# Kernel tuning notes

Measured on AMD Instinct MI355X. Metric: run time of the kernel, lower is better.

Reference implementation:

```python
import jax, jax.numpy as jnp
import numpy as np

B, L, D, H = 2, 128, 256, 256
BASE_LR = 0.01
LR_SHIFT = float(np.log(np.expm1(BASE_LR)))  # log(expm1(base_lr))


def silu_backward(x):
    s = jax.nn.silu(x)
    return s + jax.nn.sigmoid(x) * (1.0 - s)


def decay_matrix(log_g):
    # log_g: [B,L] -> M[b,l,m] = exp(sum_{i=m+1..l} log_g[b,i]) for m<=l, else 0
    n = log_g.shape[1]
    strict = jnp.tril(jnp.ones((n, n), log_g.dtype), -1)
    cum = jnp.cumsum(log_g[:, :, None] * strict, axis=1)
    return jnp.exp(cum) * jnp.tril(jnp.ones((n, n), log_g.dtype))


def setup_inputs():
    key = jax.random.key(0)
    ks = jax.random.split(key, 22)
    p = lambda k, shape: jax.random.normal(k, shape, jnp.float32) * 0.02
    inp = {
        'x': jax.random.normal(ks[0], (B, L, D), jnp.float32),
        'Wq': p(ks[1], (D, D)), 'bq': p(ks[2], (D,)),
        'Wk': p(ks[3], (D, D)), 'bk': p(ks[4], (D,)),
        'Wv': p(ks[5], (D, D)), 'bv': p(ks[6], (D,)),
        'Wlr': p(ks[7], (D, 1)), 'blr': p(ks[8], (1,)),
        'Wm': p(ks[9], (D, 1)), 'bm': p(ks[10], (1,)),
        'Wd': p(ks[11], (D, 1)), 'bd': p(ks[12], (1,)),
        'W1': p(ks[13], (B, H, D)), 'b1': p(ks[14], (B, H)),
        'W2': p(ks[15], (B, D, H)), 'b2': p(ks[16], (B, D)),
        'mW1': p(ks[17], (B, H, D)), 'mb1': p(ks[18], (B, H)),
        'mW2': p(ks[19], (B, D, H)), 'mb2': p(ks[20], (B, D)),
    }
    return inp


def reference(x, Wq, bq, Wk, bk, Wv, bv, Wlr, blr, Wm, bm, Wd, bd,
              W1, b1, W2, b2, mW1, mb1, mW2, mb2):
    query = x @ Wq + bq
    key_ = x @ Wk + bk
    value = x @ Wv + bv

    # forward through fast-weight MLP at current (chunk-start) weights
    Z1 = jnp.einsum('bhd,bld->blh', W1, key_) + b1[:, None, :]
    X2 = jax.nn.silu(Z1)
    Z2 = jnp.einsum('bdh,blh->bld', W2, X2) + b2[:, None, :]

    # per-token gradients of 0.5*||Z2 - value||^2
    grad_Z2 = Z2 - value
    grad_b2 = grad_Z2
    grad_W2 = jnp.einsum('bld,blh->bldh', grad_Z2, X2)
    grad_X2 = jnp.einsum('bld,bdh->blh', grad_Z2, W2)
    grad_Z1 = grad_X2 * silu_backward(Z1)
    grad_b1 = grad_Z1
    grad_W1 = jnp.einsum('blh,bld->blhd', grad_Z1, key_)

    lr = jax.nn.softplus((x @ Wlr).squeeze(-1) + blr + LR_SHIFT)  # [B,L]
    gW1 = grad_W1 * lr[:, :, None, None]
    gb1 = grad_b1 * lr[:, :, None]
    gW2 = grad_W2 * lr[:, :, None, None]
    gb2 = grad_b2 * lr[:, :, None]

    # momentum recurrence (decay-gated linear scan, materialized as LxL matrix)
    fc_mom = (x @ Wm).squeeze(-1) + bm  # [B,L]
    log_mom = -jax.nn.softplus(-fc_mom)
    M = decay_matrix(log_mom)  # [B,L,L]
    mom_cum = jnp.exp(jnp.cumsum(log_mom, axis=1))  # [B,L]

    mgW1 = jnp.einsum('blm,bmhd->blhd', M, gW1) - jnp.einsum('bl,bhd->blhd', mom_cum, mW1)
    mgb1 = jnp.einsum('blm,bmh->blh', M, gb1) - jnp.einsum('bl,bh->blh', mom_cum, mb1)
    mgW2 = jnp.einsum('blm,bmdh->bldh', M, gW2) - jnp.einsum('bl,bdh->bldh', mom_cum, mW2)
    mgb2 = jnp.einsum('blm,bmd->bld', M, gb2) - jnp.einsum('bl,bd->bld', mom_cum, mb2)

    # weight-decay recurrence
    log_wd = -jax.nn.softplus((x @ Wd).squeeze(-1) + bd)  # [B,L]
    Dm = decay_matrix(log_wd)
    wd_cum = jnp.exp(jnp.cumsum(log_wd, axis=1))

    W1p = jnp.einsum('blm,bmhd->blhd', Dm, mgW1) + jnp.einsum('bl,bhd->blhd', wd_cum, W1)
    b1p = jnp.einsum('blm,bmh->blh', Dm, mgb1) + jnp.einsum('bl,bh->blh', wd_cum, b1)
    W2p = jnp.einsum('blm,bmdh->bldh', Dm, mgW2) + jnp.einsum('bl,bdh->bldh', wd_cum, W2)
    b2p = jnp.einsum('blm,bmd->bld', Dm, mgb2) + jnp.einsum('bl,bd->bld', wd_cum, b2)

    # query pass through per-token updated weights
    Zq1 = jnp.einsum('blhd,bld->blh', W1p, query) + b1p
    Zq2 = jnp.einsum('bldh,blh->bld', W2p, jax.nn.silu(Zq1)) + b2p

    return (Zq2,
            W1p[:, -1], b1p[:, -1], W2p[:, -1], b2p[:, -1],
            mgW1[:, -1], mgb1[:, -1], mgW2[:, -1], mgb2[:, -1])
```

## Files before the change

kernel.cpp:

```cpp
#include <hip/hip_runtime.h>
#include <math.h>

constexpr int Bn = 2, Ln = 128, Dn = 256, Hn = 256;

#define LR_SHIFT (-4.6001660040607144f)

constexpr int OFF_Q      = 0;
constexpr int OFF_K      = 65536;
constexpr int OFF_V      = 131072;
constexpr int OFF_X2     = 196608;
constexpr int OFF_GZ1    = 262144;
constexpr int OFF_GZ2    = 327680;
constexpr int OFF_XQ     = 393216;
constexpr int OFF_KT     = 458752;
constexpr int OFF_A      = 524288;
constexpr int OFF_W1T    = 557056;
constexpr int OFF_W2T    = 688128;
constexpr int OFF_MW1T   = 819200;
constexpr int OFF_MW2T   = 950272;
constexpr int OFF_LR     = 1081344;
constexpr int OFF_PM     = 1081600;
constexpr int OFF_PD     = 1081856;
constexpr int OFF_MOMCUM = 1082112;
constexpr int OFF_WDCUM  = 1082368;
constexpr int OFF_C      = 1082624;
constexpr int OFF_LOGM   = 1082880;
constexpr int OFF_LOGWD  = 1083136;
constexpr int OFF_X2T    = 1083392;
constexpr int OFF_U1     = 1148928;
constexpr int OFF_V1     = 1214464;
constexpr int OFF_U2     = 1280000;
constexpr int OFF_V2     = 1345536;
constexpr int OFF_P2     = OFF_V;

constexpr int OUT_ZQ2  = 0;
constexpr int OUT_W1P  = 65536;
constexpr int OUT_B1P  = 196608;
constexpr int OUT_W2P  = 197120;
constexpr int OUT_B2P  = 328192;
constexpr int OUT_MGW1 = 328704;
constexpr int OUT_MGB1 = 459776;
constexpr int OUT_MGW2 = 460288;
constexpr int OUT_MGB2 = 591360;

__device__ __forceinline__ float softplus_f(float z) {
    return fmaxf(z, 0.0f) + log1pf(expf(-fabsf(z)));
}

__device__ __forceinline__ float4 fma4(float s, const float4 w, float4 a) {
    a.x += s * w.x; a.y += s * w.y; a.z += s * w.z; a.w += s * w.w; return a;
}

__device__ __forceinline__ float silu_f(float z) {
    return z / (1.0f + expf(-z));
}

__device__ __forceinline__ float dsilu_mul(float a, float z) {
    float sg = 1.0f / (1.0f + expf(-z));
    return a * (sg * (1.0f + z * (1.0f - sg)));
}

__device__ __forceinline__ void gemm_tile_16x128(
    const float* __restrict__ srcrow,
    const float* __restrict__ W,
    const float* __restrict__ bias,
    float* __restrict__ dst,
    int c0, int t, float* smem) {
    float (*xs)[260] = (float (*)[260])smem;
    for (int i = t; i < 1024; i += 256) {
        int tok = i >> 6, kq = i & 63;
        *(float4*)&xs[tok][kq * 4] = *(const float4*)(srcrow + tok * 256 + kq * 4);
    }
    __syncthreads();
    int tg = t >> 5, q = t & 31;
    int tok0 = 2 * tg, tok1 = tok0 + 1;
    int c = c0 + 4 * q;
    const float* Wp = W + c;
    float4 a0 = {0, 0, 0, 0}, a1 = {0, 0, 0, 0};
    for (int k0 = 0; k0 < 256; k0 += 16) {
        float4 wb[16];
#pragma unroll
        for (int kk = 0; kk < 16; ++kk)
            wb[kk] = *(const float4*)(Wp + (k0 + kk) * 256);
#pragma unroll
        for (int kk = 0; kk < 16; ++kk) {
            a0 = fma4(xs[tok0][k0 + kk], wb[kk], a0);
            a1 = fma4(xs[tok1][k0 + kk], wb[kk], a1);
        }
    }
    if (bias) {
        float4 bb = *(const float4*)(bias + c);
        a0.x += bb.x; a0.y += bb.y; a0.z += bb.z; a0.w += bb.w;
        a1.x += bb.x; a1.y += bb.y; a1.z += bb.z; a1.w += bb.w;
    }
    *(float4*)(dst + tok0 * 256 + c) = a0;
    *(float4*)(dst + tok1 * 256 + c) = a1;
}

__global__ __launch_bounds__(256) void prep_kernel(
    const float* __restrict__ x,
    const float* __restrict__ Wq, const float* __restrict__ bq,
    const float* __restrict__ Wk, const float* __restrict__ bk,
    const float* __restrict__ Wv, const float* __restrict__ bv,
    const float* __restrict__ Wlr, const float* __restrict__ blr,
    const float* __restrict__ Wm, const float* __restrict__ bm,
    const float* __restrict__ Wd, const float* __restrict__ bd,
    const float* __restrict__ W1, const float* __restrict__ W2,
    const float* __restrict__ mW1, const float* __restrict__ mW2,
    float* __restrict__ ws) {
    __shared__ float smem[4160];
    int id = blockIdx.x, t = threadIdx.x;
    if (id < 512) {
        int z = id >> 6; int mat = z >> 1; int b = z & 1;
        const float* src; float* dst;
        if (mat == 0)      { src = W1  + b * 65536; dst = ws + OFF_W1T  + b * 65536; }
        else if (mat == 1) { src = W2  + b * 65536; dst = ws + OFF_W2T  + b * 65536; }
        else if (mat == 2) { src = mW1 + b * 65536; dst = ws + OFF_MW1T + b * 65536; }
        else               { src = mW2 + b * 65536; dst = ws + OFF_MW2T + b * 65536; }
        float (*tile)[33] = (float (*)[33])smem;
        int tx = t & 31, ty = t >> 5;
        int tid = id & 63;
        int r0 = (tid >> 3) * 32, c0 = (tid & 7) * 32;
        for (int i = 0; i < 32; i += 8)
            tile[ty + i][tx] = src[(r0 + ty + i) * 256 + (c0 + tx)];
        __syncthreads();
        for (int i = 0; i < 32; i += 8)
            dst[(c0 + ty + i) * 256 + (r0 + tx)] = tile[tx][ty + i];
    } else if (id < 608) {
        int u = id - 512; int mat = u >> 5; int rem = u & 31;
        int c0 = (rem >> 4) * 128; int bl0 = (rem & 15) * 16;
        const float* W    = (mat == 0) ? Wq : (mat == 1) ? Wk : Wv;
        const float* bias = (mat == 0) ? bq : (mat == 1) ? bk : bv;
        int outoff = (mat == 0) ? OFF_Q : (mat == 1) ? OFF_K : OFF_V;
        gemm_tile_16x128(x + bl0 * 256, W, bias, ws + outoff + bl0 * 256, c0, t, smem);
    } else {
        int blk = id - 608;
        int ln = t & 63, wv = t >> 6;
        int bl = blk * 4 + wv;
        float4 xv = *(const float4*)(x + bl * 256 + ln * 4);
        float4 wl = *(const float4*)(Wlr + ln * 4);
        float4 wm = *(const float4*)(Wm + ln * 4);
        float4 wd = *(const float4*)(Wd + ln * 4);
        float s1 = xv.x * wl.x + xv.y * wl.y + xv.z * wl.z + xv.w * wl.w;
        float s2 = xv.x * wm.x + xv.y * wm.y + xv.z * wm.z + xv.w * wm.w;
        float s3 = xv.x * wd.x + xv.y * wd.y + xv.z * wd.z + xv.w * wd.w;
#pragma unroll
        for (int off = 32; off > 0; off >>= 1) {
            s1 += __shfl_xor(s1, off);
            s2 += __shfl_xor(s2, off);
            s3 += __shfl_xor(s3, off);
        }
        if (ln == 0) {
            ws[OFF_LR + bl]    = softplus_f(s1 + blr[0] + LR_SHIFT);
            ws[OFF_LOGM + bl]  = -softplus_f(-(s2 + bm[0]));
            ws[OFF_LOGWD + bl] = -softplus_f(s3 + bd[0]);
        }
    }
}

__global__ __launch_bounds__(256) void mid_kernel(
    const float* __restrict__ W2nat, const float* __restrict__ b1,
    const float* __restrict__ b2, const float* __restrict__ mb1,
    float* __restrict__ ws) {
    __shared__ float smem[8320];
    int id = blockIdx.x, t = threadIdx.x;
    if (id < 32) {
        int bl0 = id * 8;
        int b = bl0 >> 7;
        float (*ks)[260] = (float (*)[260])smem;
        float (*zs)[260] = (float (*)[260])(smem + 2080);
        float (*as)[260] = (float (*)[260])(smem + 4160);
        float (*gs)[260] = (float (*)[260])(smem + 6240);
        for (int i = t; i < 512; i += 256) {
            int tok = i >> 6, kq = i & 63;
            *(float4*)&ks[tok][kq * 4] =
                *(const float4*)(ws + OFF_K + (bl0 + tok) * 256 + kq * 4);
        }
        __syncthreads();
        int tok = t >> 5, q = t & 31;
        int c = 4 * q, c2 = c + 128;
        {
            const float* W1t = ws + OFF_W1T + b * 65536;
            float4 a0 = {0, 0, 0, 0}, a1 = {0, 0, 0, 0};
            for (int k0 = 0; k0 < 256; k0 += 8) {
                float4 w0[8], w1[8];
#pragma unroll
                for (int kk = 0; kk < 8; ++kk) {
                    w0[kk] = *(const float4*)(W1t + (k0 + kk) * 256 + c);
                    w1[kk] = *(const float4*)(W1t + (k0 + kk) * 256 + c2);
                }
#pragma unroll
                for (int kk = 0; kk < 8; ++kk) {
                    float kv = ks[tok][k0 + kk];
                    a0 = fma4(kv, w0[kk], a0);
                    a1 = fma4(kv, w1[kk], a1);
                }
            }
            float4 bb0 = *(const float4*)(b1 + b * 256 + c);
            float4 bb1 = *(const float4*)(b1 + b * 256 + c2);
            float4 z0 = {a0.x + bb0.x, a0.y + bb0.y, a0.z + bb0.z, a0.w + bb0.w};
            float4 z1 = {a1.x + bb1.x, a1.y + bb1.y, a1.z + bb1.z, a1.w + bb1.w};
            *(float4*)&zs[tok][c]  = z0;
            *(float4*)&zs[tok][c2] = z1;
            float4 s0 = {silu_f(z0.x), silu_f(z0.y), silu_f(z0.z), silu_f(z0.w)};
            float4 s1 = {silu_f(z1.x), silu_f(z1.y), silu_f(z1.z), silu_f(z1.w)};
            *(float4*)&as[tok][c]  = s0;
            *(float4*)&as[tok][c2] = s1;
            *(float4*)(ws + OFF_X2 + (bl0 + tok) * 256 + c)  = s0;
            *(float4*)(ws + OFF_X2 + (bl0 + tok) * 256 + c2) = s1;
        }
        __syncthreads();
        {
            int l0b = bl0 & 127;
            float v0[8], v1[8];
#pragma unroll
            for (int j = 0; j < 8; ++j) { v0[j] = ks[j][t]; v1[j] = as[j][t]; }
            float* KTp  = ws + OFF_KT  + b * 32768 + t * 128 + l0b;
            float* X2Tp = ws + OFF_X2T + b * 32768 + t * 128 + l0b;
            float4 p0 = {v0[0], v0[1], v0[2], v0[3]};
            float4 p1 = {v0[4], v0[5], v0[6], v0[7]};
            *(float4*)KTp = p0; *(float4*)(KTp + 4) = p1;
            float4 r0 = {v1[0], v1[1], v1[2], v1[3]};
            float4 r1 = {v1[4], v1[5], v1[6], v1[7]};
            *(float4*)X2Tp = r0; *(float4*)(X2Tp + 4) = r1;
        }
        {
            const float* W2t = ws + OFF_W2T + b * 65536;
            float4 a0 = {0, 0, 0, 0}, a1 = {0, 0, 0, 0};
            for (int k0 = 0; k0 < 256; k0 += 8) {
                float4 w0[8], w1[8];
#pragma unroll
                for (int kk = 0; kk < 8; ++kk) {
                    w0[kk] = *(const float4*)(W2t + (k0 + kk) * 256 + c);
                    w1[kk] = *(const float4*)(W2t + (k0 + kk) * 256 + c2);
                }
#pragma unroll
                for (int kk = 0; kk < 8; ++kk) {
                    float xv = as[tok][k0 + kk];
                    a0 = fma4(xv, w0[kk], a0);
                    a1 = fma4(xv, w1[kk], a1);
                }
            }
            float4 bb0 = *(const float4*)(b2 + b * 256 + c);
            float4 bb1 = *(const float4*)(b2 + b * 256 + c2);
            float4 v0 = *(const float4*)(ws + OFF_V + (bl0 + tok) * 256 + c);
            float4 v1 = *(const float4*)(ws + OFF_V + (bl0 + tok) * 256 + c2);
            float4 g0 = {a0.x + bb0.x - v0.x, a0.y + bb0.y - v0.y,
                         a0.z + bb0.z - v0.z, a0.w + bb0.w - v0.w};
            float4 g1 = {a1.x + bb1.x - v1.x, a1.y + bb1.y - v1.y,
                         a1.z + bb1.z - v1.z, a1.w + bb1.w - v1.w};
            *(float4*)&gs[tok][c]  = g0;
            *(float4*)&gs[tok][c2] = g1;
            *(float4*)(ws + OFF_GZ2 + (bl0 + tok) * 256 + c)  = g0;
            *(float4*)(ws + OFF_GZ2 + (bl0 + tok) * 256 + c2) = g1;
        }
        __syncthreads();
        {
            const float* W2n = W2nat + b * 65536;
            float4 a0 = {0, 0, 0, 0}, a1 = {0, 0, 0, 0};
            for (int k0 = 0; k0 < 256; k0 += 8) {
                float4 w0[8], w1[8];
#pragma unroll
                for (int kk = 0; kk < 8; ++kk) {
                    w0[kk] = *(const float4*)(W2n + (k0 + kk) * 256 + c);
                    w1[kk] = *(const float4*)(W2n + (k0 + kk) * 256 + c2);
                }
#pragma unroll
                for (int kk = 0; kk < 8; ++kk) {
                    float gv = gs[tok][k0 + kk];
                    a0 = fma4(gv, w0[kk], a0);
                    a1 = fma4(gv, w1[kk], a1);
                }
            }
            float4 z0 = *(float4*)&zs[tok][c];
            float4 z1 = *(float4*)&zs[tok][c2];
            float4 g0 = {dsilu_mul(a0.x, z0.x), dsilu_mul(a0.y, z0.y),
                         dsilu_mul(a0.z, z0.z), dsilu_mul(a0.w, z0.w)};
            float4 g1 = {dsilu_mul(a1.x, z1.x), dsilu_mul(a1.y, z1.y),
                         dsilu_mul(a1.z, z1.z), dsilu_mul(a1.w, z1.w)};
            *(float4*)(ws + OFF_GZ1 + (bl0 + tok) * 256 + c)  = g0;
            *(float4*)(ws + OFF_GZ1 + (bl0 + tok) * 256 + c2) = g1;
        }
    } else if (id < 288) {
        int u = id - 32; int b = u >> 7; int l = u & 127;
        float* sm = smem;
        float* sd = smem + 128;
        float* se = smem + 256;
        if (t < 128) {
            sm[t] = ws[OFF_LOGM + b * Ln + t];
            sd[t] = ws[OFF_LOGWD + b * Ln + t];
        }
        __syncthreads();
        for (int off = 1; off < 128; off <<= 1) {
            float am = 0.0f, ad = 0.0f;
            if (t < 128 && t >= off) { am = sm[t - off]; ad = sd[t - off]; }
            __syncthreads();
            if (t < 128) { sm[t] += am; sd[t] += ad; }
            __syncthreads();
        }
        if (l == 0) {
            if (t < 128) {
                float pm = sm[t], pd = sd[t];
                ws[OFF_PM + b * Ln + t] = pm;
                ws[OFF_PD + b * Ln + t] = pd;
                ws[OFF_MOMCUM + b * Ln + t] = expf(pm);
                ws[OFF_WDCUM + b * Ln + t]  = expf(pd);
                se[t] = expf(pm - pd);
            }
            __syncthreads();
            for (int off = 1; off < 128; off <<= 1) {
                float a = 0.0f;
                if (t < 128 && t >= off) a = se[t - off];
                __syncthreads();
                if (t < 128) se[t] += a;
                __syncthreads();
            }
            if (t < 128) ws[OFF_C + b * Ln + t] = expf(sd[t]) * se[t];
        }
        if (t < 128) {
            int m1 = t;
            float a = 0.0f;
            if (m1 <= l) {
                float pdl = sd[l], pmm1 = sm[m1];
                float s = 0.0f;
                for (int m = m1; m <= l; ++m)
                    s += expf((pdl - sd[m]) + (sm[m] - pmm1));
                a = s;
            }
            ws[OFF_A + (b * Ln + l) * Ln + m1] = a;
        }
    } else {
        int u = id - 288; int mat = u >> 5; int rem = u & 31;
        int c0 = (rem >> 4) * 128; int bl0 = (rem & 15) * 16;
        int b = bl0 >> 7;
        const float* W    = ws + (mat == 0 ? OFF_W1T : OFF_MW1T) + b * 65536;
        const float* bias = (mat == 0 ? b1 : mb1) + b * 256;
        float* dst = ws + (mat == 0 ? OFF_U1 : OFF_V1) + bl0 * 256;
        gemm_tile_16x128(ws + OFF_Q + bl0 * 256, W, bias, dst, c0, t, smem);
    }
}

__global__ __launch_bounds__(256) void fin1_kernel(
    const float* __restrict__ W1, const float* __restrict__ mW1,
    const float* __restrict__ W2nat, const float* __restrict__ mW2,
    const float* __restrict__ b1, const float* __restrict__ mb1,
    const float* __restrict__ b2, const float* __restrict__ mb2,
    float* __restrict__ out, float* __restrict__ ws) {
    __shared__ float smem[6400];
    int id = blockIdx.x, t = threadIdx.x;
    if (id < 64) {
        int b = id >> 5; int rem = id & 31;
        int l0 = (rem >> 1) * 8; int ct = rem & 1;
        int bl0 = b * 128 + l0; int c0 = ct * 128;
        float (*qs)[260] = (float (*)[260])smem;
        float (*ps)[132] = (float (*)[132])(smem + 2080);
        for (int i = t; i < 512; i += 256) {
            int tok = i >> 6, kq = i & 63;
            *(float4*)&qs[tok][kq * 4] =
                *(const float4*)(ws + OFF_Q + (bl0 + tok) * 256 + kq * 4);
        }
        __syncthreads();
        int tok = t >> 5;
        int l = l0 + tok;
        {
            int mq = t & 31, m0 = 4 * mq;
            const float* KT = ws + OFF_KT + b * 32768 + m0;
            float4 s = {0, 0, 0, 0};
            for (int d0 = 0; d0 < 256; d0 += 16) {
                float4 kb[16];
#pragma unroll
                for (int kk = 0; kk < 16; ++kk)
                    kb[kk] = *(const float4*)(KT + (d0 + kk) * 128);
#pragma unroll
                for (int kk = 0; kk < 16; ++kk)
                    s = fma4(qs[tok][d0 + kk], kb[kk], s);
            }
            float4 A4 = *(const float4*)(ws + OFF_A + (b * 128 + l) * 128 + m0);
            float4 L4 = *(const float4*)(ws + OFF_LR + b * 128 + m0);
            float4 pv;
            pv.x = (m0 + 0 <= l) ? A4.x * L4.x * (1.0f + s.x) : 0.0f;
            pv.y = (m0 + 1 <= l) ? A4.y * L4.y * (1.0f + s.y) : 0.0f;
            pv.z = (m0 + 2 <= l) ? A4.z * L4.z * (1.0f + s.z) : 0.0f;
            pv.w = (m0 + 3 <= l) ? A4.w * L4.w * (1.0f + s.w) : 0.0f;
            *(float4*)&ps[tok][m0] = pv;
        }
        __syncthreads();
        {
            int q = t & 31;
            int c = c0 + 4 * q;
            float cl  = ws[OFF_C + b * 128 + l];
            float wdc = ws[OFF_WDCUM + b * 128 + l];
            float4 p = {0, 0, 0, 0};
            const float* G = ws + OFF_GZ1 + b * 32768 + c;
            int mmax = l0 + 8;
            for (int m0 = 0; m0 < mmax; m0 += 8) {
                float4 gb[8];
#pragma unroll
                for (int kk = 0; kk < 8; ++kk)
                    gb[kk] = *(const float4*)(G + (m0 + kk) * 256);
#pragma unroll
                for (int kk = 0; kk < 8; ++kk)
                    p = fma4(ps[tok][m0 + kk], gb[kk], p);
            }
            float4 u4 = *(const float4*)(ws + OFF_U1 + (bl0 + tok) * 256 + c);
            float4 v4 = *(const float4*)(ws + OFF_V1 + (bl0 + tok) * 256 + c);
            float4 o;
            o.x = silu_f(p.x - cl * v4.x + wdc * u4.x);
            o.y = silu_f(p.y - cl * v4.y + wdc * u4.y);
            o.z = silu_f(p.z - cl * v4.z + wdc * u4.z);
            o.w = silu_f(p.w - cl * v4.w + wdc * u4.w);
            *(float4*)(ws + OFF_XQ + (bl0 + tok) * 256 + c) = o;
        }
    } else if (id < 1088) {
        int u = id - 64; int z = u >> 8; int rem = u & 255;
        int b = z >> 1; int fam = z & 1;
        int i0 = (rem >> 4) * 16, j0 = (rem & 15) * 16;
        float* wa = smem;
        float* wm = smem + 128;
        float (*LA)[16] = (float (*)[16])(smem + 256);
        float (*LM)[16] = (float (*)[16])(smem + 256 + 2048);
        float (*R)[16]  = (float (*)[16])(smem + 256 + 4096);
        const float* lr = ws + OFF_LR + b * Ln;
        const float* Pm = ws + OFF_PM + b * Ln;
        const float* Arow = ws + OFF_A + (b * Ln + Ln - 1) * Ln;
        if (t < 128) {
            wa[t] = Arow[t] * lr[t];
            wm[t] = expf(Pm[Ln - 1] - Pm[t]) * lr[t];
        }
        const float* left  = ws + (fam == 0 ? OFF_GZ1 : OFF_GZ2) + b * Ln * 256;
        const float* right = ws + (fam == 0 ? OFF_K   : OFF_X2 ) + b * Ln * 256;
        __syncthreads();
        for (int e = t; e < 2048; e += 256) {
            int m = e >> 4, i = e & 15;
            float lv = left[m * 256 + i0 + i];
            LA[m][i] = wa[m] * lv;
            LM[m][i] = wm[m] * lv;
            R[m][i]  = right[m * 256 + j0 + i];
        }
        __syncthreads();
        int tx = t & 15, ty = t >> 4;
        float accA = 0.0f, accM = 0.0f;
#pragma unroll 4
        for (int m = 0; m < 128; ++m) {
            accA += LA[m][ty] * R[m][tx];
            accM += LM[m][ty] * R[m][tx];
        }
        float c_last  = ws[OFF_C + b * Ln + Ln - 1];
        float wd_last = ws[OFF_WDCUM + b * Ln + Ln - 1];
        float mc_last = ws[OFF_MOMCUM + b * Ln + Ln - 1];
        int i = i0 + ty, j = j0 + tx;
        const float* base1 = (fam == 0 ? W1 : W2nat) + b * 65536;
        const float* basem = (fam == 0 ? mW1 : mW2) + b * 65536;
        float b1v = base1[i * 256 + j], bmv = basem[i * 256 + j];
        int op = (fam == 0 ? OUT_W1P : OUT_W2P) + (b * 256 + i) * 256 + j;
        int om = (fam == 0 ? OUT_MGW1 : OUT_MGW2) + (b * 256 + i) * 256 + j;
        out[op] = accA - c_last * bmv + wd_last * b1v;
        out[om] = accM - mc_last * bmv;
    } else {
        int b = id - 1088;
        float* wa = smem;
        float* wm = smem + 128;
        if (t < 128) {
            wa[t] = ws[OFF_A + (b * Ln + Ln - 1) * Ln + t] * ws[OFF_LR + b * Ln + t];
            wm[t] = expf(ws[OFF_PM + b * Ln + Ln - 1] - ws[OFF_PM + b * Ln + t]) *
                    ws[OFF_LR + b * Ln + t];
        }
        __syncthreads();
        const float* gz1 = ws + OFF_GZ1 + b * Ln * 256;
        const float* gz2 = ws + OFF_GZ2 + b * Ln * 256;
        float sA1 = 0, sM1 = 0, sA2 = 0, sM2 = 0;
#pragma unroll 4
        for (int m = 0; m < 128; ++m) {
            float g1 = gz1[m * 256 + t], g2 = gz2[m * 256 + t];
            sA1 += wa[m] * g1; sM1 += wm[m] * g1;
            sA2 += wa[m] * g2; sM2 += wm[m] * g2;
        }
        float c_last  = ws[OFF_C + b * Ln + Ln - 1];
        float wd_last = ws[OFF_WDCUM + b * Ln + Ln - 1];
        float mc_last = ws[OFF_MOMCUM + b * Ln + Ln - 1];
        out[OUT_B1P + b * 256 + t]  = sA1 - c_last * mb1[b * 256 + t] + wd_last * b1[b * 256 + t];
        out[OUT_MGB1 + b * 256 + t] = sM1 - mc_last * mb1[b * 256 + t];
        out[OUT_B2P + b * 256 + t]  = sA2 - c_last * mb2[b * 256 + t] + wd_last * b2[b * 256 + t];
        out[OUT_MGB2 + b * 256 + t] = sM2 - mc_last * mb2[b * 256 + t];
    }
}

__global__ __launch_bounds__(256) void fin2_kernel(
    const float* __restrict__ b2, const float* __restrict__ mb2,
    float* __restrict__ ws) {
    __shared__ float smem[4160];
    int id = blockIdx.x, t = threadIdx.x;
    if (id < 32) {
        int b = id >> 4; int l0 = (id & 15) * 8; int bl0 = b * 128 + l0;
        float (*qs)[260] = (float (*)[260])smem;
        for (int i = t; i < 512; i += 256) {
            int tok = i >> 6, kq = i & 63;
            *(float4*)&qs[tok][kq * 4] =
                *(const float4*)(ws + OFF_XQ + (bl0 + tok) * 256 + kq * 4);
        }
        __syncthreads();
        int tok = t >> 5, mq = t & 31, m0 = 4 * mq;
        int l = l0 + tok;
        const float* X2T = ws + OFF_X2T + b * 32768 + m0;
        float4 s = {0, 0, 0, 0};
        for (int d0 = 0; d0 < 256; d0 += 16) {
            float4 kb[16];
#pragma unroll
            for (int kk = 0; kk < 16; ++kk)
                kb[kk] = *(const float4*)(X2T + (d0 + kk) * 128);
#pragma unroll
            for (int kk = 0; kk < 16; ++kk)
                s = fma4(qs[tok][d0 + kk], kb[kk], s);
        }
        float4 A4 = *(const float4*)(ws + OFF_A + (b * 128 + l) * 128 + m0);
        float4 L4 = *(const float4*)(ws + OFF_LR + b * 128 + m0);
        float4 pv;
        pv.x = (m0 + 0 <= l) ? A4.x * L4.x * (1.0f + s.x) : 0.0f;
        pv.y = (m0 + 1 <= l) ? A4.y * L4.y * (1.0f + s.y) : 0.0f;
        pv.z = (m0 + 2 <= l) ? A4.z * L4.z * (1.0f + s.z) : 0.0f;
        pv.w = (m0 + 3 <= l) ? A4.w * L4.w * (1.0f + s.w) : 0.0f;
        *(float4*)(ws + OFF_P2 + (b * 128 + l) * 128 + m0) = pv;
    } else {
        int u = id - 32; int mat = u >> 5; int rem = u & 31;
        int c0 = (rem >> 4) * 128; int bl0 = (rem & 15) * 16;
        int b = bl0 >> 7;
        const float* W    = ws + (mat == 0 ? OFF_W2T : OFF_MW2T) + b * 65536;
        const float* bias = (mat == 0 ? b2 : mb2) + b * 256;
        float* dst = ws + (mat == 0 ? OFF_U2 : OFF_V2) + bl0 * 256;
        gemm_tile_16x128(ws + OFF_XQ + bl0 * 256, W, bias, dst, c0, t, smem);
    }
}

__global__ __launch_bounds__(256) void fin3_kernel(
    float* __restrict__ out, float* __restrict__ ws) {
    __shared__ float smem[1056];
    int id = blockIdx.x, t = threadIdx.x;
    int b = id >> 5; int rem = id & 31;
    int l0 = (rem >> 1) * 8; int ct = rem & 1;
    int bl0 = b * 128 + l0; int c0 = ct * 128;
    float (*ps)[132] = (float (*)[132])smem;
    {
        int tok = t >> 5, mq = t & 31;
        *(float4*)&ps[tok][mq * 4] =
            *(const float4*)(ws + OFF_P2 + (b * 128 + l0 + tok) * 128 + mq * 4);
    }
    __syncthreads();
    int tok = t >> 5, q = t & 31;
    int l = l0 + tok;
    int c = c0 + 4 * q;
    float cl  = ws[OFF_C + b * 128 + l];
    float wdc = ws[OFF_WDCUM + b * 128 + l];
    float4 p = {0, 0, 0, 0};
    const float* G = ws + OFF_GZ2 + b * 32768 + c;
    int mmax = l0 + 8;
    for (int m0 = 0; m0 < mmax; m0 += 8) {
        float4 gb[8];
#pragma unroll
        for (int kk = 0; kk < 8; ++kk)
            gb[kk] = *(const float4*)(G + (m0 + kk) * 256);
#pragma unroll
        for (int kk = 0; kk < 8; ++kk)
            p = fma4(ps[tok][m0 + kk], gb[kk], p);
    }
    float4 u4 = *(const float4*)(ws + OFF_U2 + (bl0 + tok) * 256 + c);
    float4 v4 = *(const float4*)(ws + OFF_V2 + (bl0 + tok) * 256 + c);
    float4 o;
    o.x = p.x - cl * v4.x + wdc * u4.x;
    o.y = p.y - cl * v4.y + wdc * u4.y;
    o.z = p.z - cl * v4.z + wdc * u4.z;
    o.w = p.w - cl * v4.w + wdc * u4.w;
    *(float4*)(out + OUT_ZQ2 + (bl0 + tok) * 256 + c) = o;
}

extern "C" void kernel_launch(void* const* d_in, const int* in_sizes, int n_in,
                              void* d_out, int out_size, void* d_ws, size_t ws_size,
                              hipStream_t stream) {
    const float* x   = (const float*)d_in[0];
    const float* Wq  = (const float*)d_in[1];
    const float* bq  = (const float*)d_in[2];
    const float* Wk  = (const float*)d_in[3];
    const float* bk  = (const float*)d_in[4];
    const float* Wv  = (const float*)d_in[5];
    const float* bv  = (const float*)d_in[6];
    const float* Wlr = (const float*)d_in[7];
    const float* blr = (const float*)d_in[8];
    const float* Wm  = (const float*)d_in[9];
    const float* bm  = (const float*)d_in[10];
    const float* Wd  = (const float*)d_in[11];
    const float* bd  = (const float*)d_in[12];
    const float* W1  = (const float*)d_in[13];
    const float* b1  = (const float*)d_in[14];
    const float* W2  = (const float*)d_in[15];
    const float* b2  = (const float*)d_in[16];
    const float* mW1 = (const float*)d_in[17];
    const float* mb1 = (const float*)d_in[18];
    const float* mW2 = (const float*)d_in[19];
    const float* mb2 = (const float*)d_in[20];
    float* ws  = (float*)d_ws;
    float* out = (float*)d_out;

    prep_kernel<<<672, 256, 0, stream>>>(x, Wq, bq, Wk, bk, Wv, bv,
                                         Wlr, blr, Wm, bm, Wd, bd,
                                         W1, W2, mW1, mW2, ws);
    mid_kernel<<<352, 256, 0, stream>>>(W2, b1, b2, mb1, ws);
    fin1_kernel<<<1090, 256, 0, stream>>>(W1, mW1, W2, mW2,
                                          b1, mb1, b2, mb2, out, ws);
    fin2_kernel<<<96, 256, 0, stream>>>(b2, mb2, ws);
    fin3_kernel<<<64, 256, 0, stream>>>(out, ws);
}
```

Before: 216.4 us.

## Replace five-kernel pipeline with cooperative persistent megakernel using grid syncs

Merges the separate prep/mid/fin kernels into a single persistent cooperative kernel that walks seven phases, with grid-wide synchronisation between them. Work is redistributed into per-phase units (score, combine, last-weight, bias reductions) over a grid capped by occupancy. The goal is to remove launch overhead and tail idle time between the five launches. The cost is grid-sync latency, lower parallelism per phase, and a fallback that launches the kernel once per phase when cooperative launch is unavailable.

```diff
diff --git a/kernel.cpp b/kernel.cpp
--- a/kernel.cpp
+++ b/kernel.cpp
@@ -1,5 +1,8 @@
 #include <hip/hip_runtime.h>
+#include <hip/hip_cooperative_groups.h>
 #include <math.h>
+
+namespace cg = cooperative_groups;
 
 constexpr int Bn = 2, Ln = 128, Dn = 256, Hn = 256;
 
@@ -31,6 +34,7 @@
 constexpr int OFF_V1     = 1214464;
 constexpr int OFF_U2     = 1280000;
 constexpr int OFF_V2     = 1345536;
+constexpr int OFF_P1     = 1411072;
 constexpr int OFF_P2     = OFF_V;
 
 constexpr int OUT_ZQ2  = 0;
@@ -43,506 +47,129 @@
 constexpr int OUT_MGW2 = 460288;
 constexpr int OUT_MGB2 = 591360;
 
+struct KParams {
+    const float *x;
+    const float *Wq, *bq, *Wk, *bk, *Wv, *bv;
+    const float *Wlr, *blr, *Wm, *bm, *Wd, *bd;
+    const float *W1, *b1, *W2, *b2, *mW1, *mb1, *mW2, *mb2;
+    float *out, *ws;
+};
+
 __device__ __forceinline__ float softplus_f(float z) {
     return fmaxf(z, 0.0f) + log1pf(expf(-fabsf(z)));
 }
-
 __device__ __forceinline__ float4 fma4(float s, const float4 w, float4 a) {
     a.x += s * w.x; a.y += s * w.y; a.z += s * w.z; a.w += s * w.w; return a;
 }
-
 __device__ __forceinline__ float silu_f(float z) {
     return z / (1.0f + expf(-z));
 }
-
 __device__ __forceinline__ float dsilu_mul(float a, float z) {
     float sg = 1.0f / (1.0f + expf(-z));
     return a * (sg * (1.0f + z * (1.0f - sg)));
 }
 
-__device__ __forceinline__ void gemm_tile_16x128(
-    const float* __restrict__ srcrow,
-    const float* __restrict__ W,
-    const float* __restrict__ bias,
-    float* __restrict__ dst,
-    int c0, int t, float* smem) {
-    float (*xs)[260] = (float (*)[260])smem;
-    for (int i = t; i < 1024; i += 256) {
-        int tok = i >> 6, kq = i & 63;
-        *(float4*)&xs[tok][kq * 4] = *(const float4*)(srcrow + tok * 256 + kq * 4);
-    }
-    __syncthreads();
-    int tg = t >> 5, q = t & 31;
-    int tok0 = 2 * tg, tok1 = tok0 + 1;
-    int c = c0 + 4 * q;
-    const float* Wp = W + c;
-    float4 a0 = {0, 0, 0, 0}, a1 = {0, 0, 0, 0};
+__device__ __forceinline__ void stage8(const float* __restrict__ src,
+                                       float (*xs)[260], int t) {
+#pragma unroll
+    for (int i = 0; i < 2; ++i) {
+        int e = t + i * 256; int tok = e >> 6, kq = e & 63;
+        *(float4*)&xs[tok][kq * 4] = *(const float4*)(src + tok * 256 + kq * 4);
+    }
+}
+
+__device__ __forceinline__ float4 dot256(const float (*xs)[260], int tok,
+                                         const float* __restrict__ Wc, int ldw) {
+    float4 a = {0, 0, 0, 0};
     for (int k0 = 0; k0 < 256; k0 += 16) {
         float4 wb[16];
 #pragma unroll
         for (int kk = 0; kk < 16; ++kk)
-            wb[kk] = *(const float4*)(Wp + (k0 + kk) * 256);
+            wb[kk] = *(const float4*)(Wc + (k0 + kk) * ldw);
 #pragma unroll
-        for (int kk = 0; kk < 16; ++kk) {
-            a0 = fma4(xs[tok0][k0 + kk], wb[kk], a0);
-            a1 = fma4(xs[tok1][k0 + kk], wb[kk], a1);
-        }
-    }
-    if (bias) {
-        float4 bb = *(const float4*)(bias + c);
-        a0.x += bb.x; a0.y += bb.y; a0.z += bb.z; a0.w += bb.w;
-        a1.x += bb.x; a1.y += bb.y; a1.z += bb.z; a1.w += bb.w;
-    }
-    *(float4*)(dst + tok0 * 256 + c) = a0;
-    *(float4*)(dst + tok1 * 256 + c) = a1;
-}
-
-__global__ __launch_bounds__(256) void prep_kernel(
-    const float* __restrict__ x,
-    const float* __restrict__ Wq, const float* __restrict__ bq,
-    const float* __restrict__ Wk, const float* __restrict__ bk,
-    const float* __restrict__ Wv, const float* __restrict__ bv,
-    const float* __restrict__ Wlr, const float* __restrict__ blr,
-    const float* __restrict__ Wm, const float* __restrict__ bm,
-    const float* __restrict__ Wd, const float* __restrict__ bd,
-    const float* __restrict__ W1, const float* __restrict__ W2,
-    const float* __restrict__ mW1, const float* __restrict__ mW2,
-    float* __restrict__ ws) {
-    __shared__ float smem[4160];
-    int id = blockIdx.x, t = threadIdx.x;
-    if (id < 512) {
-        int z = id >> 6; int mat = z >> 1; int b = z & 1;
-        const float* src; float* dst;
-        if (mat == 0)      { src = W1  + b * 65536; dst = ws + OFF_W1T  + b * 65536; }
-        else if (mat == 1) { src = W2  + b * 65536; dst = ws + OFF_W2T  + b * 65536; }
-        else if (mat == 2) { src = mW1 + b * 65536; dst = ws + OFF_MW1T + b * 65536; }
-        else               { src = mW2 + b * 65536; dst = ws + OFF_MW2T + b * 65536; }
-        float (*tile)[33] = (float (*)[33])smem;
-        int tx = t & 31, ty = t >> 5;
-        int tid = id & 63;
-        int r0 = (tid >> 3) * 32, c0 = (tid & 7) * 32;
-        for (int i = 0; i < 32; i += 8)
-            tile[ty + i][tx] = src[(r0 + ty + i) * 256 + (c0 + tx)];
-        __syncthreads();
-        for (int i = 0; i < 32; i += 8)
-            dst[(c0 + ty + i) * 256 + (r0 + tx)] = tile[tx][ty + i];
-    } else if (id < 608) {
-        int u = id - 512; int mat = u >> 5; int rem = u & 31;
-        int c0 = (rem >> 4) * 128; int bl0 = (rem & 15) * 16;
-        const float* W    = (mat == 0) ? Wq : (mat == 1) ? Wk : Wv;
-        const float* bias = (mat == 0) ? bq : (mat == 1) ? bk : bv;
-        int outoff = (mat == 0) ? OFF_Q : (mat == 1) ? OFF_K : OFF_V;
-        gemm_tile_16x128(x + bl0 * 256, W, bias, ws + outoff + bl0 * 256, c0, t, smem);
-    } else {
-        int blk = id - 608;
-        int ln = t & 63, wv = t >> 6;
-        int bl = blk * 4 + wv;
-        float4 xv = *(const float4*)(x + bl * 256 + ln * 4);
-        float4 wl = *(const float4*)(Wlr + ln * 4);
-        float4 wm = *(const float4*)(Wm + ln * 4);
-        float4 wd = *(const float4*)(Wd + ln * 4);
-        float s1 = xv.x * wl.x + xv.y * wl.y + xv.z * wl.z + xv.w * wl.w;
-        float s2 = xv.x * wm.x + xv.y * wm.y + xv.z * wm.z + xv.w * wm.w;
-        float s3 = xv.x * wd.x + xv.y * wd.y + xv.z * wd.z + xv.w * wd.w;
-#pragma unroll
-        for (int off = 32; off > 0; off >>= 1) {
-            s1 += __shfl_xor(s1, off);
-            s2 += __shfl_xor(s2, off);
-            s3 += __shfl_xor(s3, off);
-        }
-        if (ln == 0) {
-            ws[OFF_LR + bl]    = softplus_f(s1 + blr[0] + LR_SHIFT);
-            ws[OFF_LOGM + bl]  = -softplus_f(-(s2 + bm[0]));
-            ws[OFF_LOGWD + bl] = -softplus_f(s3 + bd[0]);
-        }
-    }
-}
-
-__global__ __launch_bounds__(256) void mid_kernel(
-    const float* __restrict__ W2nat, const float* __restrict__ b1,
-    const float* __restrict__ b2, const float* __restrict__ mb1,
-    float* __restrict__ ws) {
-    __shared__ float smem[8320];
-    int id = blockIdx.x, t = threadIdx.x;
-    if (id < 32) {
-        int bl0 = id * 8;
-        int b = bl0 >> 7;
-        float (*ks)[260] = (float (*)[260])smem;
-        float (*zs)[260] = (float (*)[260])(smem + 2080);
-        float (*as)[260] = (float (*)[260])(smem + 4160);
-        float (*gs)[260] = (float (*)[260])(smem + 6240);
-        for (int i = t; i < 512; i += 256) {
-            int tok = i >> 6, kq = i & 63;
-            *(float4*)&ks[tok][kq * 4] =
-                *(const float4*)(ws + OFF_K + (bl0 + tok) * 256 + kq * 4);
-        }
-        __syncthreads();
-        int tok = t >> 5, q = t & 31;
-        int c = 4 * q, c2 = c + 128;
-        {
-            const float* W1t = ws + OFF_W1T + b * 65536;
-            float4 a0 = {0, 0, 0, 0}, a1 = {0, 0, 0, 0};
-            for (int k0 = 0; k0 < 256; k0 += 8) {
-                float4 w0[8], w1[8];
-#pragma unroll
-                for (int kk = 0; kk < 8; ++kk) {
-                    w0[kk] = *(const float4*)(W1t + (k0 + kk) * 256 + c);
-                    w1[kk] = *(const float4*)(W1t + (k0 + kk) * 256 + c2);
-                }
-#pragma unroll
-                for (int kk = 0; kk < 8; ++kk) {
-                    float kv = ks[tok][k0 + kk];
-                    a0 = fma4(kv, w0[kk], a0);
-                    a1 = fma4(kv, w1[kk], a1);
-                }
-            }
-            float4 bb0 = *(const float4*)(b1 + b * 256 + c);
-            float4 bb1 = *(const float4*)(b1 + b * 256 + c2);
-            float4 z0 = {a0.x + bb0.x, a0.y + bb0.y, a0.z + bb0.z, a0.w + bb0.w};
-            float4 z1 = {a1.x + bb1.x, a1.y + bb1.y, a1.z + bb1.z, a1.w + bb1.w};
-            *(float4*)&zs[tok][c]  = z0;
-            *(float4*)&zs[tok][c2] = z1;
-            float4 s0 = {silu_f(z0.x), silu_f(z0.y), silu_f(z0.z), silu_f(z0.w)};
-            float4 s1 = {silu_f(z1.x), silu_f(z1.y), silu_f(z1.z), silu_f(z1.w)};
-            *(float4*)&as[tok][c]  = s0;
-            *(float4*)&as[tok][c2] = s1;
-            *(float4*)(ws + OFF_X2 + (bl0 + tok) * 256 + c)  = s0;
-            *(float4*)(ws + OFF_X2 + (bl0 + tok) * 256 + c2) = s1;
-        }
-        __syncthreads();
-        {
-            int l0b = bl0 & 127;
-            float v0[8], v1[8];
-#pragma unroll
-            for (int j = 0; j < 8; ++j) { v0[j] = ks[j][t]; v1[j] = as[j][t]; }
-            float* KTp  = ws + OFF_KT  + b * 32768 + t * 128 + l0b;
-            float* X2Tp = ws + OFF_X2T + b * 32768 + t * 128 + l0b;
-            float4 p0 = {v0[0], v0[1], v0[2], v0[3]};
-            float4 p1 = {v0[4], v0[5], v0[6], v0[7]};
-            *(float4*)KTp = p0; *(float4*)(KTp + 4) = p1;
-            float4 r0 = {v1[0], v1[1], v1[2], v1[3]};
-            float4 r1 = {v1[4], v1[5], v1[6], v1[7]};
-            *(float4*)X2Tp = r0; *(float4*)(X2Tp + 4) = r1;
-        }
-        {
-            const float* W2t = ws + OFF_W2T + b * 65536;
-            float4 a0 = {0, 0, 0, 0}, a1 = {0, 0, 0, 0};
-            for (int k0 = 0; k0 < 256; k0 += 8) {
-                float4 w0[8], w1[8];
-#pragma unroll
-                for (int kk = 0; kk < 8; ++kk) {
-                    w0[kk] = *(const float4*)(W2t + (k0 + kk) * 256 + c);
-                    w1[kk] = *(const float4*)(W2t + (k0 + kk) * 256 + c2);
-                }
-#pragma unroll
-                for (int kk = 0; kk < 8; ++kk) {
-                    float xv = as[tok][k0 + kk];
-                    a0 = fma4(xv, w0[kk], a0);
-                    a1 = fma4(xv, w1[kk], a1);
-                }
-            }
-            float4 bb0 = *(const float4*)(b2 + b * 256 + c);
-            float4 bb1 = *(const float4*)(b2 + b * 256 + c2);
-            float4 v0 = *(const float4*)(ws + OFF_V + (bl0 + tok) * 256 + c);
-            float4 v1 = *(const float4*)(ws + OFF_V + (bl0 + tok) * 256 + c2);
-            float4 g0 = {a0.x + bb0.x - v0.x, a0.y + bb0.y - v0.y,
-                         a0.z + bb0.z - v0.z, a0.w + bb0.w - v0.w};
-            float4 g1 = {a1.x + bb1.x - v1.x, a1.y + bb1.y - v1.y,
-                         a1.z + bb1.z - v1.z, a1.w + bb1.w - v1.w};
-            *(float4*)&gs[tok][c]  = g0;
-            *(float4*)&gs[tok][c2] = g1;
-            *(float4*)(ws + OFF_GZ2 + (bl0 + tok) * 256 + c)  = g0;
-            *(float4*)(ws + OFF_GZ2 + (bl0 + tok) * 256 + c2) = g1;
-        }
-        __syncthreads();
-        {
-            const float* W2n = W2nat + b * 65536;
-            float4 a0 = {0, 0, 0, 0}, a1 = {0, 0, 0, 0};
-            for (int k0 = 0; k0 < 256; k0 += 8) {
-                float4 w0[8], w1[8];
-#pragma unroll
-                for (int kk = 0; kk < 8; ++kk) {
-                    w0[kk] = *(const float4*)(W2n + (k0 + kk) * 256 + c);
-                    w1[kk] = *(const float4*)(W2n + (k0 + kk) * 256 + c2);
-                }
-#pragma unroll
-                for (int kk = 0; kk < 8; ++kk) {
-                    float gv = gs[tok][k0 + kk];
-                    a0 = fma4(gv, w0[kk], a0);
-                    a1 = fma4(gv, w1[kk], a1);
-                }
-            }
-            float4 z0 = *(float4*)&zs[tok][c];
-            float4 z1 = *(float4*)&zs[tok][c2];
-            float4 g0 = {dsilu_mul(a0.x, z0.x), dsilu_mul(a0.y, z0.y),
-                         dsilu_mul(a0.z, z0.z), dsilu_mul(a0.w, z0.w)};
-            float4 g1 = {dsilu_mul(a1.x, z1.x), dsilu_mul(a1.y, z1.y),
-                         dsilu_mul(a1.z, z1.z), dsilu_mul(a1.w, z1.w)};
-            *(float4*)(ws + OFF_GZ1 + (bl0 + tok) * 256 + c)  = g0;
-            *(float4*)(ws + OFF_GZ1 + (bl0 + tok) * 256 + c2) = g1;
-        }
-    } else if (id < 288) {
-        int u = id - 32; int b = u >> 7; int l = u & 127;
-        float* sm = smem;
-        float* sd = smem + 128;
-        float* se = smem + 256;
-        if (t < 128) {
-            sm[t] = ws[OFF_LOGM + b * Ln + t];
-            sd[t] = ws[OFF_LOGWD + b * Ln + t];
-        }
-        __syncthreads();
-        for (int off = 1; off < 128; off <<= 1) {
-            float am = 0.0f, ad = 0.0f;
-            if (t < 128 && t >= off) { am = sm[t - off]; ad = sd[t - off]; }
-            __syncthreads();
-            if (t < 128) { sm[t] += am; sd[t] += ad; }
-            __syncthreads();
-        }
-        if (l == 0) {
-            if (t < 128) {
-                float pm = sm[t], pd = sd[t];
-                ws[OFF_PM + b * Ln + t] = pm;
-                ws[OFF_PD + b * Ln + t] = pd;
-                ws[OFF_MOMCUM + b * Ln + t] = expf(pm);
-                ws[OFF_WDCUM + b * Ln + t]  = expf(pd);
-                se[t] = expf(pm - pd);
-            }
-            __syncthreads();
-            for (int off = 1; off < 128; off <<= 1) {
-                float a = 0.0f;
-                if (t < 128 && t >= off) a = se[t - off];
-                __syncthreads();
-                if (t < 128) se[t] += a;
-                __syncthreads();
-            }
-            if (t < 128) ws[OFF_C + b * Ln + t] = expf(sd[t]) * se[t];
-        }
-        if (t < 128) {
-            int m1 = t;
-            float a = 0.0f;
-            if (m1 <= l) {
-                float pdl = sd[l], pmm1 = sm[m1];
-                float s = 0.0f;
-                for (int m = m1; m <= l; ++m)
-                    s += expf((pdl - sd[m]) + (sm[m] - pmm1));
-                a = s;
-            }
-            ws[OFF_A + (b * Ln + l) * Ln + m1] = a;
-        }
-    } else {
-        int u = id - 288; int mat = u >> 5; int rem = u & 31;
-        int c0 = (rem >> 4) * 128; int bl0 = (rem & 15) * 16;
-        int b = bl0 >> 7;
-        const float* W    = ws + (mat == 0 ? OFF_W1T : OFF_MW1T) + b * 65536;
-        const float* bias = (mat == 0 ? b1 : mb1) + b * 256;
-        float* dst = ws + (mat == 0 ? OFF_U1 : OFF_V1) + bl0 * 256;
-        gemm_tile_16x128(ws + OFF_Q + bl0 * 256, W, bias, dst, c0, t, smem);
-    }
-}
-
-__global__ __launch_bounds__(256) void fin1_kernel(
-    const float* __restrict__ W1, const float* __restrict__ mW1,
-    const float* __restrict__ W2nat, const float* __restrict__ mW2,
-    const float* __restrict__ b1, const float* __restrict__ mb1,
-    const float* __restrict__ b2, const float* __restrict__ mb2,
-    float* __restrict__ out, float* __restrict__ ws) {
-    __shared__ float smem[6400];
-    int id = blockIdx.x, t = threadIdx.x;
-    if (id < 64) {
-        int b = id >> 5; int rem = id & 31;
-        int l0 = (rem >> 1) * 8; int ct = rem & 1;
-        int bl0 = b * 128 + l0; int c0 = ct * 128;
-        float (*qs)[260] = (float (*)[260])smem;
-        float (*ps)[132] = (float (*)[132])(smem + 2080);
-        for (int i = t; i < 512; i += 256) {
-            int tok = i >> 6, kq = i & 63;
-            *(float4*)&qs[tok][kq * 4] =
-                *(const float4*)(ws + OFF_Q + (bl0 + tok) * 256 + kq * 4);
-        }
-        __syncthreads();
-        int tok = t >> 5;
-        int l = l0 + tok;
-        {
-            int mq = t & 31, m0 = 4 * mq;
-            const float* KT = ws + OFF_KT + b * 32768 + m0;
-            float4 s = {0, 0, 0, 0};
-            for (int d0 = 0; d0 < 256; d0 += 16) {
-                float4 kb[16];
-#pragma unroll
-                for (int kk = 0; kk < 16; ++kk)
-                    kb[kk] = *(const float4*)(KT + (d0 + kk) * 128);
-#pragma unroll
-                for (int kk = 0; kk < 16; ++kk)
-                    s = fma4(qs[tok][d0 + kk], kb[kk], s);
-            }
-            float4 A4 = *(const float4*)(ws + OFF_A + (b * 128 + l) * 128 + m0);
-            float4 L4 = *(const float4*)(ws + OFF_LR + b * 128 + m0);
-            float4 pv;
-            pv.x = (m0 + 0 <= l) ? A4.x * L4.x * (1.0f + s.x) : 0.0f;
-            pv.y = (m0 + 1 <= l) ? A4.y * L4.y * (1.0f + s.y) : 0.0f;
-            pv.z = (m0 + 2 <= l) ? A4.z * L4.z * (1.0f + s.z) : 0.0f;
-            pv.w = (m0 + 3 <= l) ? A4.w * L4.w * (1.0f + s.w) : 0.0f;
-            *(float4*)&ps[tok][m0] = pv;
-        }
-        __syncthreads();
-        {
-            int q = t & 31;
-            int c = c0 + 4 * q;
-            float cl  = ws[OFF_C + b * 128 + l];
-            float wdc = ws[OFF_WDCUM + b * 128 + l];
-            float4 p = {0, 0, 0, 0};
-            const float* G = ws + OFF_GZ1 + b * 32768 + c;
-            int mmax = l0 + 8;
-            for (int m0 = 0; m0 < mmax; m0 += 8) {
-                float4 gb[8];
-#pragma unroll
-                for (int kk = 0; kk < 8; ++kk)
-                    gb[kk] = *(const float4*)(G + (m0 + kk) * 256);
-#pragma unroll
-                for (int kk = 0; kk < 8; ++kk)
-                    p = fma4(ps[tok][m0 + kk], gb[kk], p);
-            }
-            float4 u4 = *(const float4*)(ws + OFF_U1 + (bl0 + tok) * 256 + c);
-            float4 v4 = *(const float4*)(ws + OFF_V1 + (bl0 + tok) * 256 + c);
-            float4 o;
-            o.x = silu_f(p.x - cl * v4.x + wdc * u4.x);
-            o.y = silu_f(p.y - cl * v4.y + wdc * u4.y);
-            o.z = silu_f(p.z - cl * v4.z + wdc * u4.z);
-            o.w = silu_f(p.w - cl * v4.w + wdc * u4.w);
-            *(float4*)(ws + OFF_XQ + (bl0 + tok) * 256 + c) = o;
-        }
-    } else if (id < 1088) {
-        int u = id - 64; int z = u >> 8; int rem = u & 255;
-        int b = z >> 1; int fam = z & 1;
-        int i0 = (rem >> 4) * 16, j0 = (rem & 15) * 16;
-        float* wa = smem;
-        float* wm = smem + 128;
-        float (*LA)[16] = (float (*)[16])(smem + 256);
-        float (*LM)[16] = (float (*)[16])(smem + 256 + 2048);
-        float (*R)[16]  = (float (*)[16])(smem + 256 + 4096);
-        const float* lr = ws + OFF_LR + b * Ln;
-        const float* Pm = ws + OFF_PM + b * Ln;
-        const float* Arow = ws + OFF_A + (b * Ln + Ln - 1) * Ln;
-        if (t < 128) {
-            wa[t] = Arow[t] * lr[t];
-            wm[t] = expf(Pm[Ln - 1] - Pm[t]) * lr[t];
-        }
-        const float* left  = ws + (fam == 0 ? OFF_GZ1 : OFF_GZ2) + b * Ln * 256;
-        const float* right = ws + (fam == 0 ? OFF_K   : OFF_X2 ) + b * Ln * 256;
-        __syncthreads();
-        for (int e = t; e < 2048; e += 256) {
-            int m = e >> 4, i = e & 15;
-            float lv = left[m * 256 + i0 + i];
-            LA[m][i] = wa[m] * lv;
-            LM[m][i] = wm[m] * lv;
-            R[m][i]  = right[m * 256 + j0 + i];
-        }
-        __syncthreads();
-        int tx = t & 15, ty = t >> 4;
-        float accA = 0.0f, accM = 0.0f;
+        for (int kk = 0; kk < 16; ++kk)
+            a = fma4(xs[tok][k0 + kk], wb[kk], a);
+    }
+    return a;
+}
+
+__device__ __forceinline__ void lastw_unit(const KParams& p, float* smem, int t,
+                                           int b, int fam, int i0, int j0) {
+    const float* ws = p.ws;
+    float* wa = smem;
+    float* wm = smem + 128;
+    float (*LA)[16] = (float (*)[16])(smem + 256);
+    float (*LM)[16] = (float (*)[16])(smem + 256 + 2048);
+    float (*R)[16]  = (float (*)[16])(smem + 256 + 4096);
+    const float* lr = ws + OFF_LR + b * Ln;
+    const float* Pm = ws + OFF_PM + b * Ln;
+    const float* Arow = ws + OFF_A + (b * Ln + Ln - 1) * Ln;
+    if (t < 128) {
+        wa[t] = Arow[t] * lr[t];
+        wm[t] = expf(Pm[Ln - 1] - Pm[t]) * lr[t];
+    }
+    const float* left  = ws + (fam == 0 ? OFF_GZ1 : OFF_GZ2) + b * Ln * 256;
+    const float* right = ws + (fam == 0 ? OFF_K   : OFF_X2 ) + b * Ln * 256;
+    __syncthreads();
+    for (int e = t; e < 2048; e += 256) {
+        int m = e >> 4, i = e & 15;
+        float lv = left[m * 256 + i0 + i];
+        LA[m][i] = wa[m] * lv;
+        LM[m][i] = wm[m] * lv;
+        R[m][i]  = right[m * 256 + j0 + i];
+    }
+    __syncthreads();
+    int tx = t & 15, ty = t >> 4;
+    float accA = 0.0f, accM = 0.0f;
 #pragma unroll 4
-        for (int m = 0; m < 128; ++m) {
-            accA += LA[m][ty] * R[m][tx];
-            accM += LM[m][ty] * R[m][tx];
-        }
-        float c_last  = ws[OFF_C + b * Ln + Ln - 1];
-        float wd_last = ws[OFF_WDCUM + b * Ln + Ln - 1];
-        float mc_last = ws[OFF_MOMCUM + b * Ln + Ln - 1];
-        int i = i0 + ty, j = j0 + tx;
-        const float* base1 = (fam == 0 ? W1 : W2nat) + b * 65536;
-        const float* basem = (fam == 0 ? mW1 : mW2) + b * 65536;
-        float b1v = base1[i * 256 + j], bmv = basem[i * 256 + j];
-        int op = (fam == 0 ? OUT_W1P : OUT_W2P) + (b * 256 + i) * 256 + j;
-        int om = (fam == 0 ? OUT_MGW1 : OUT_MGW2) + (b * 256 + i) * 256 + j;
-        out[op] = accA - c_last * bmv + wd_last * b1v;
-        out[om] = accM - mc_last * bmv;
-    } else {
-        int b = id - 1088;
-        float* wa = smem;
-        float* wm = smem + 128;
-        if (t < 128) {
-            wa[t] = ws[OFF_A + (b * Ln + Ln - 1) * Ln + t] * ws[OFF_LR + b * Ln + t];
-            wm[t] = expf(ws[OFF_PM + b * Ln + Ln - 1] - ws[OFF_PM + b * Ln + t]) *
-                    ws[OFF_LR + b * Ln + t];
-        }
-        __syncthreads();
-        const float* gz1 = ws + OFF_GZ1 + b * Ln * 256;
-        const float* gz2 = ws + OFF_GZ2 + b * Ln * 256;
-        float sA1 = 0, sM1 = 0, sA2 = 0, sM2 = 0;
-#pragma unroll 4
-        for (int m = 0; m < 128; ++m) {
-            float g1 = gz1[m * 256 + t], g2 = gz2[m * 256 + t];
-            sA1 += wa[m] * g1; sM1 += wm[m] * g1;
-            sA2 += wa[m] * g2; sM2 += wm[m] * g2;
-        }
-        float c_last  = ws[OFF_C + b * Ln + Ln - 1];
-        float wd_last = ws[OFF_WDCUM + b * Ln + Ln - 1];
-        float mc_last = ws[OFF_MOMCUM + b * Ln + Ln - 1];
-        out[OUT_B1P + b * 256 + t]  = sA1 - c_last * mb1[b * 256 + t] + wd_last * b1[b * 256 + t];
-        out[OUT_MGB1 + b * 256 + t] = sM1 - mc_last * mb1[b * 256 + t];
-        out[OUT_B2P + b * 256 + t]  = sA2 - c_last * mb2[b * 256 + t] + wd_last * b2[b * 256 + t];
-        out[OUT_MGB2 + b * 256 + t] = sM2 - mc_last * mb2[b * 256 + t];
-    }
-}
-
-__global__ __launch_bounds__(256) void fin2_kernel(
-    const float* __restrict__ b2, const float* __restrict__ mb2,
-    float* __restrict__ ws) {
-    __shared__ float smem[4160];
-    int id = blockIdx.x, t = threadIdx.x;
-    if (id < 32) {
-        int b = id >> 4; int l0 = (id & 15) * 8; int bl0 = b * 128 + l0;
-        float (*qs)[260] = (float (*)[260])smem;
-        for (int i = t; i < 512; i += 256) {
-            int tok = i >> 6, kq = i & 63;
-            *(float4*)&qs[tok][kq * 4] =
-                *(const float4*)(ws + OFF_XQ + (bl0 + tok) * 256 + kq * 4);
-        }
-        __syncthreads();
-        int tok = t >> 5, mq = t & 31, m0 = 4 * mq;
-        int l = l0 + tok;
-        const float* X2T = ws + OFF_X2T + b * 32768 + m0;
-        float4 s = {0, 0, 0, 0};
-        for (int d0 = 0; d0 < 256; d0 += 16) {
-            float4 kb[16];
-#pragma unroll
-            for (int kk = 0; kk < 16; ++kk)
-                kb[kk] = *(const float4*)(X2T + (d0 + kk) * 128);
-#pragma unroll
-            for (int kk = 0; kk < 16; ++kk)
-                s = fma4(qs[tok][d0 + kk], kb[kk], s);
-        }
-        float4 A4 = *(const float4*)(ws + OFF_A + (b * 128 + l) * 128 + m0);
-        float4 L4 = *(const float4*)(ws + OFF_LR + b * 128 + m0);
-        float4 pv;
-        pv.x = (m0 + 0 <= l) ? A4.x * L4.x * (1.0f + s.x) : 0.0f;
-        pv.y = (m0 + 1 <= l) ? A4.y * L4.y * (1.0f + s.y) : 0.0f;
-        pv.z = (m0 + 2 <= l) ? A4.z * L4.z * (1.0f + s.z) : 0.0f;
-        pv.w = (m0 + 3 <= l) ? A4.w * L4.w * (1.0f + s.w) : 0.0f;
-        *(float4*)(ws + OFF_P2 + (b * 128 + l) * 128 + m0) = pv;
-    } else {
-        int u = id - 32; int mat = u >> 5; int rem = u & 31;
-        int c0 = (rem >> 4) * 128; int bl0 = (rem & 15) * 16;
-        int b = bl0 >> 7;
-        const float* W    = ws + (mat == 0 ? OFF_W2T : OFF_MW2T) + b * 65536;
-        const float* bias = (mat == 0 ? b2 : mb2) + b * 256;
-        float* dst = ws + (mat == 0 ? OFF_U2 : OFF_V2) + bl0 * 256;
-        gemm_tile_16x128(ws + OFF_XQ + bl0 * 256, W, bias, dst, c0, t, smem);
-    }
-}
-
-__global__ __launch_bounds__(256) void fin3_kernel(
-    float* __restrict__ out, float* __restrict__ ws) {
-    __shared__ float smem[1056];
-    int id = blockIdx.x, t = threadIdx.x;
-    int b = id >> 5; int rem = id & 31;
-    int l0 = (rem >> 1) * 8; int ct = rem & 1;
-    int bl0 = b * 128 + l0; int c0 = ct * 128;
+    for (int m = 0; m < 128; ++m) {
+        accA += LA[m][ty] * R[m][tx];
+        accM += LM[m][ty] * R[m][tx];
+    }
+    float c_last  = ws[OFF_C + b * Ln + Ln - 1];
+    float wd_last = ws[OFF_WDCUM + b * Ln + Ln - 1];
+    float mc_last = ws[OFF_MOMCUM + b * Ln + Ln - 1];
+    int i = i0 + ty, j = j0 + tx;
+    const float* base1 = (fam == 0 ? p.W1 : p.W2) + b * 65536;
+    const float* basem = (fam == 0 ? p.mW1 : p.mW2) + b * 65536;
+    float b1v = base1[i * 256 + j], bmv = basem[i * 256 + j];
+    int op = (fam == 0 ? OUT_W1P : OUT_W2P) + (b * 256 + i) * 256 + j;
+    int om = (fam == 0 ? OUT_MGW1 : OUT_MGW2) + (b * 256 + i) * 256 + j;
+    p.out[op] = accA - c_last * bmv + wd_last * b1v;
+    p.out[om] = accM - mc_last * bmv;
+}
+
+__device__ __forceinline__ void score_unit(const KParams& p, float* smem, int t,
+                                           int b, int l0, int srcoff, int btoff,
+                                           int poff) {
+    const float* ws = p.ws;
+    float (*qs)[260] = (float (*)[260])smem;
+    stage8(ws + srcoff + (b * 128 + l0) * 256, qs, t);
+    __syncthreads();
+    int tok = t >> 5, mq = t & 31, m0 = 4 * mq;
+    int l = l0 + tok;
+    float4 s = dot256(qs, tok, ws + btoff + b * 32768 + m0, 128);
+    float4 A4 = *(const float4*)(ws + OFF_A + (b * 128 + l) * 128 + m0);
+    float4 L4 = *(const float4*)(ws + OFF_LR + b * 128 + m0);
+    float4 pv;
+    pv.x = (m0 + 0 <= l) ? A4.x * L4.x * (1.0f + s.x) : 0.0f;
+    pv.y = (m0 + 1 <= l) ? A4.y * L4.y * (1.0f + s.y) : 0.0f;
+    pv.z = (m0 + 2 <= l) ? A4.z * L4.z * (1.0f + s.z) : 0.0f;
+    pv.w = (m0 + 3 <= l) ? A4.w * L4.w * (1.0f + s.w) : 0.0f;
+    *(float4*)(p.ws + poff + b * 16384 + l * 128 + m0) = pv;
+}
+
+__device__ __forceinline__ void combine_unit(const KParams& p, float* smem, int t,
+                                             int b, int l0, int c0, int poff,
+                                             int goff, int uoff, int voff,
+                                             int dooutsilu, float* dst) {
+    const float* ws = p.ws;
+    int bl0 = b * 128 + l0;
     float (*ps)[132] = (float (*)[132])smem;
     {
         int tok = t >> 5, mq = t & 31;
         *(float4*)&ps[tok][mq * 4] =
-            *(const float4*)(ws + OFF_P2 + (b * 128 + l0 + tok) * 128 + mq * 4);
+            *(const float4*)(ws + poff + b * 16384 + (l0 + tok) * 128 + mq * 4);
     }
     __syncthreads();
     int tok = t >> 5, q = t & 31;
@@ -550,8 +177,8 @@
     int c = c0 + 4 * q;
     float cl  = ws[OFF_C + b * 128 + l];
     float wdc = ws[OFF_WDCUM + b * 128 + l];
-    float4 p = {0, 0, 0, 0};
-    const float* G = ws + OFF_GZ2 + b * 32768 + c;
+    float4 acc = {0, 0, 0, 0};
+    const float* G = ws + goff + b * 32768 + c;
     int mmax = l0 + 8;
     for (int m0 = 0; m0 < mmax; m0 += 8) {
         float4 gb[8];
@@ -560,51 +187,343 @@
             gb[kk] = *(const float4*)(G + (m0 + kk) * 256);
 #pragma unroll
         for (int kk = 0; kk < 8; ++kk)
-            p = fma4(ps[tok][m0 + kk], gb[kk], p);
-    }
-    float4 u4 = *(const float4*)(ws + OFF_U2 + (bl0 + tok) * 256 + c);
-    float4 v4 = *(const float4*)(ws + OFF_V2 + (bl0 + tok) * 256 + c);
+            acc = fma4(ps[tok][m0 + kk], gb[kk], acc);
+    }
+    float4 u4 = *(const float4*)(ws + uoff + (bl0 + tok) * 256 + c);
+    float4 v4 = *(const float4*)(ws + voff + (bl0 + tok) * 256 + c);
     float4 o;
-    o.x = p.x - cl * v4.x + wdc * u4.x;
-    o.y = p.y - cl * v4.y + wdc * u4.y;
-    o.z = p.z - cl * v4.z + wdc * u4.z;
-    o.w = p.w - cl * v4.w + wdc * u4.w;
-    *(float4*)(out + OUT_ZQ2 + (bl0 + tok) * 256 + c) = o;
+    o.x = acc.x - cl * v4.x + wdc * u4.x;
+    o.y = acc.y - cl * v4.y + wdc * u4.y;
+    o.z = acc.z - cl * v4.z + wdc * u4.z;
+    o.w = acc.w - cl * v4.w + wdc * u4.w;
+    if (dooutsilu) {
+        o.x = silu_f(o.x); o.y = silu_f(o.y); o.z = silu_f(o.z); o.w = silu_f(o.w);
+    }
+    *(float4*)(dst + (bl0 + tok) * 256 + c) = o;
+}
+
+__global__ __launch_bounds__(256, 2) void mega_kernel(KParams p, int lo, int hi) {
+    __shared__ float smem[6400];
+    const int t = threadIdx.x;
+    float* ws = p.ws;
+
+    for (int ph = lo; ph <= hi; ++ph) {
+        if (ph > lo) cg::this_grid().sync();
+
+        if (ph == 0) {
+            for (int u = blockIdx.x; u < 768; u += gridDim.x) {
+                if (u < 512) {
+                    int z = u >> 6; int mat = z >> 1; int b = z & 1;
+                    const float* src; float* dst;
+                    if (mat == 0)      { src = p.W1  + b * 65536; dst = ws + OFF_W1T  + b * 65536; }
+                    else if (mat == 1) { src = p.W2  + b * 65536; dst = ws + OFF_W2T  + b * 65536; }
+                    else if (mat == 2) { src = p.mW1 + b * 65536; dst = ws + OFF_MW1T + b * 65536; }
+                    else               { src = p.mW2 + b * 65536; dst = ws + OFF_MW2T + b * 65536; }
+                    float (*tile)[33] = (float (*)[33])smem;
+                    int tx = t & 31, ty = t >> 5;
+                    int tid = u & 63;
+                    int r0 = (tid >> 3) * 32, c0 = (tid & 7) * 32;
+                    for (int i = 0; i < 32; i += 8)
+                        tile[ty + i][tx] = src[(r0 + ty + i) * 256 + (c0 + tx)];
+                    __syncthreads();
+                    for (int i = 0; i < 32; i += 8)
+                        dst[(c0 + ty + i) * 256 + (r0 + tx)] = tile[tx][ty + i];
+                } else if (u < 704) {
+                    int v = u - 512; int mat = v >> 6; int r = v & 63;
+                    int ct = r >> 5, tt = r & 31;
+                    int bl0 = tt * 8, c0 = ct * 128;
+                    const float* W    = (mat == 0) ? p.Wq : (mat == 1) ? p.Wk : p.Wv;
+                    const float* bias = (mat == 0) ? p.bq : (mat == 1) ? p.bk : p.bv;
+                    int outoff = (mat == 0) ? OFF_Q : (mat == 1) ? OFF_K : OFF_V;
+                    float (*xs)[260] = (float (*)[260])smem;
+                    stage8(p.x + bl0 * 256, xs, t);
+                    __syncthreads();
+                    int tok = t >> 5, q = t & 31;
+                    int c = c0 + 4 * q;
+                    float4 a = dot256(xs, tok, W + c, 256);
+                    float4 bb = *(const float4*)(bias + c);
+                    a.x += bb.x; a.y += bb.y; a.z += bb.z; a.w += bb.w;
+                    *(float4*)(ws + outoff + (bl0 + tok) * 256 + c) = a;
+                    if (mat == 1) {
+                        int b = bl0 >> 7, l = (bl0 & 127) + tok;
+                        float* KT = ws + OFF_KT + b * 32768 + l;
+                        KT[(c + 0) * 128] = a.x; KT[(c + 1) * 128] = a.y;
+                        KT[(c + 2) * 128] = a.z; KT[(c + 3) * 128] = a.w;
+                    }
+                } else {
+                    int blk = u - 704;
+                    int ln = t & 63, wv = t >> 6;
+                    int bl = blk * 4 + wv;
+                    float4 xv = *(const float4*)(p.x + bl * 256 + ln * 4);
+                    float4 wl = *(const float4*)(p.Wlr + ln * 4);
+                    float4 wm = *(const float4*)(p.Wm + ln * 4);
+                    float4 wd = *(const float4*)(p.Wd + ln * 4);
+                    float s1 = xv.x * wl.x + xv.y * wl.y + xv.z * wl.z + xv.w * wl.w;
+                    float s2 = xv.x * wm.x + xv.y * wm.y + xv.z * wm.z + xv.w * wm.w;
+                    float s3 = xv.x * wd.x + xv.y * wd.y + xv.z * wd.z + xv.w * wd.w;
+#pragma unroll
+                    for (int off = 32; off > 0; off >>= 1) {
+                        s1 += __shfl_xor(s1, off);
+                        s2 += __shfl_xor(s2, off);
+                        s3 += __shfl_xor(s3, off);
+                    }
+                    if (ln == 0) {
+                        ws[OFF_LR + bl]    = softplus_f(s1 + p.blr[0] + LR_SHIFT);
+                        ws[OFF_LOGM + bl]  = -softplus_f(-(s2 + p.bm[0]));
+                        ws[OFF_LOGWD + bl] = -softplus_f(s3 + p.bd[0]);
+                    }
+                }
+                __syncthreads();
+            }
+        } else if (ph == 1) {
+            for (int u = blockIdx.x; u < 448; u += gridDim.x) {
+                if (u < 64) {
+                    int tt = u >> 1, ct = u & 1;
+                    int bl0 = tt * 8, c0 = ct * 128, b = bl0 >> 7;
+                    float (*xs)[260] = (float (*)[260])smem;
+                    stage8(ws + OFF_K + bl0 * 256, xs, t);
+                    __syncthreads();
+                    int tok = t >> 5, q = t & 31;
+                    int c = c0 + 4 * q;
+                    float4 a = dot256(xs, tok, ws + OFF_W1T + b * 65536 + c, 256);
+                    float4 bb = *(const float4*)(p.b1 + b * 256 + c);
+                    float4 z = {a.x + bb.x, a.y + bb.y, a.z + bb.z, a.w + bb.w};
+                    *(float4*)(ws + OFF_GZ1 + (bl0 + tok) * 256 + c) = z;
+                    float4 s = {silu_f(z.x), silu_f(z.y), silu_f(z.z), silu_f(z.w)};
+                    *(float4*)(ws + OFF_X2 + (bl0 + tok) * 256 + c) = s;
+                    int l = (bl0 & 127) + tok;
+                    float* X2T = ws + OFF_X2T + b * 32768 + l;
+                    X2T[(c + 0) * 128] = s.x; X2T[(c + 1) * 128] = s.y;
+                    X2T[(c + 2) * 128] = s.z; X2T[(c + 3) * 128] = s.w;
+                } else if (u < 320) {
+                    int w = u - 64; int b = w >> 7; int l = w & 127;
+                    float* sm = smem;
+                    float* sd = smem + 128;
+                    float* se = smem + 256;
+                    if (t < 128) {
+                        sm[t] = ws[OFF_LOGM + b * Ln + t];
+                        sd[t] = ws[OFF_LOGWD + b * Ln + t];
+                    }
+                    __syncthreads();
+                    for (int off = 1; off < 128; off <<= 1) {
+                        float am = 0.0f, ad = 0.0f;
+                        if (t < 128 && t >= off) { am = sm[t - off]; ad = sd[t - off]; }
+                        __syncthreads();
+                        if (t < 128) { sm[t] += am; sd[t] += ad; }
+                        __syncthreads();
+                    }
+                    if (l == 0) {
+                        if (t < 128) {
+                            float pm = sm[t], pd = sd[t];
+                            ws[OFF_PM + b * Ln + t] = pm;
+                            ws[OFF_PD + b * Ln + t] = pd;
+                            ws[OFF_MOMCUM + b * Ln + t] = expf(pm);
+                            ws[OFF_WDCUM + b * Ln + t]  = expf(pd);
+                            se[t] = expf(pm - pd);
+                        }
+                        __syncthreads();
+                        for (int off = 1; off < 128; off <<= 1) {
+                            float a = 0.0f;
+                            if (t < 128 && t >= off) a = se[t - off];
+                            __syncthreads();
+                            if (t < 128) se[t] += a;
+                            __syncthreads();
+                        }
+                        if (t < 128) ws[OFF_C + b * Ln + t] = expf(sd[t]) * se[t];
+                    }
+                    if (t < 128) {
+                        int m1 = t;
+                        float a = 0.0f;
+                        if (m1 <= l) {
+                            float pdl = sd[l], pmm1 = sm[m1];
+                            float s = 0.0f;
+                            for (int m = m1; m <= l; ++m)
+                                s += expf((pdl - sd[m]) + (sm[m] - pmm1));
+                            a = s;
+                        }
+                        ws[OFF_A + (b * Ln + l) * Ln + m1] = a;
+                    }
+                } else {
+                    int w = u - 320;
+                    int tt = w >> 2, ct = (w >> 1) & 1, mat = w & 1;
+                    int bl0 = tt * 8, c0 = ct * 128, b = bl0 >> 7;
+                    float (*xs)[260] = (float (*)[260])smem;
+                    stage8(ws + OFF_Q + bl0 * 256, xs, t);
+                    __syncthreads();
+                    int tok = t >> 5, q = t & 31;
+                    int c = c0 + 4 * q;
+                    const float* W = ws + (mat ? OFF_MW1T : OFF_W1T) + b * 65536 + c;
+                    const float* bias = (mat ? p.mb1 : p.b1) + b * 256 + c;
+                    float4 a = dot256(xs, tok, W, 256);
+                    float4 bb = *(const float4*)bias;
+                    a.x += bb.x; a.y += bb.y; a.z += bb.z; a.w += bb.w;
+                    *(float4*)(ws + (mat ? OFF_V1 : OFF_U1) + (bl0 + tok) * 256 + c) = a;
+                }
+                __syncthreads();
+            }
+        } else if (ph == 2) {
+            for (int u = blockIdx.x; u < 96; u += gridDim.x) {
+                if (u < 64) {
+                    int tt = u >> 1, ct = u & 1;
+                    int bl0 = tt * 8, c0 = ct * 128, b = bl0 >> 7;
+                    float (*xs)[260] = (float (*)[260])smem;
+                    stage8(ws + OFF_X2 + bl0 * 256, xs, t);
+                    __syncthreads();
+                    int tok = t >> 5, q = t & 31;
+                    int c = c0 + 4 * q;
+                    float4 a = dot256(xs, tok, ws + OFF_W2T + b * 65536 + c, 256);
+                    float4 bb = *(const float4*)(p.b2 + b * 256 + c);
+                    float4 v4 = *(const float4*)(ws + OFF_V + (bl0 + tok) * 256 + c);
+                    float4 g = {a.x + bb.x - v4.x, a.y + bb.y - v4.y,
+                                a.z + bb.z - v4.z, a.w + bb.w - v4.w};
+                    *(float4*)(ws + OFF_GZ2 + (bl0 + tok) * 256 + c) = g;
+                } else {
+                    int w = u - 64; int b = w >> 4; int l0 = (w & 15) * 8;
+                    score_unit(p, smem, t, b, l0, OFF_Q, OFF_KT, OFF_P1);
+                }
+                __syncthreads();
+            }
+        } else if (ph == 3) {
+            for (int u = blockIdx.x; u < 576; u += gridDim.x) {
+                if (u < 64) {
+                    int tt = u >> 1, ct = u & 1;
+                    int bl0 = tt * 8, c0 = ct * 128, b = bl0 >> 7;
+                    float (*xs)[260] = (float (*)[260])smem;
+                    stage8(ws + OFF_GZ2 + bl0 * 256, xs, t);
+                    __syncthreads();
+                    int tok = t >> 5, q = t & 31;
+                    int c = c0 + 4 * q;
+                    float4 a = dot256(xs, tok, p.W2 + b * 65536 + c, 256);
+                    float4 z = *(const float4*)(ws + OFF_GZ1 + (bl0 + tok) * 256 + c);
+                    float4 g = {dsilu_mul(a.x, z.x), dsilu_mul(a.y, z.y),
+                                dsilu_mul(a.z, z.z), dsilu_mul(a.w, z.w)};
+                    *(float4*)(ws + OFF_GZ1 + (bl0 + tok) * 256 + c) = g;
+                } else {
+                    int w = u - 64; int b = w >> 8; int rem = w & 255;
+                    lastw_unit(p, smem, t, b, 1, (rem >> 4) * 16, (rem & 15) * 16);
+                }
+                __syncthreads();
+            }
+        } else if (ph == 4) {
+            for (int u = blockIdx.x; u < 578; u += gridDim.x) {
+                if (u < 64) {
+                    int tt = u >> 1, ct = u & 1;
+                    int b = tt >> 4, l0 = (tt & 15) * 8;
+                    combine_unit(p, smem, t, b, l0, ct * 128, OFF_P1, OFF_GZ1,
+                                 OFF_U1, OFF_V1, 1, ws + OFF_XQ);
+                } else if (u < 576) {
+                    int w = u - 64; int b = w >> 8; int rem = w & 255;
+                    lastw_unit(p, smem, t, b, 0, (rem >> 4) * 16, (rem & 15) * 16);
+                } else {
+                    int b = u - 576;
+                    float* wa = smem;
+                    float* wm = smem + 128;
+                    if (t < 128) {
+                        wa[t] = ws[OFF_A + (b * Ln + Ln - 1) * Ln + t] * ws[OFF_LR + b * Ln + t];
+                        wm[t] = expf(ws[OFF_PM + b * Ln + Ln - 1] - ws[OFF_PM + b * Ln + t]) *
+                                ws[OFF_LR + b * Ln + t];
+                    }
+                    __syncthreads();
+                    const float* gz1 = ws + OFF_GZ1 + b * Ln * 256;
+                    const float* gz2 = ws + OFF_GZ2 + b * Ln * 256;
+                    float sA1 = 0, sM1 = 0, sA2 = 0, sM2 = 0;
+#pragma unroll 4
+                    for (int m = 0; m < 128; ++m) {
+                        float g1 = gz1[m * 256 + t], g2 = gz2[m * 256 + t];
+                        sA1 += wa[m] * g1; sM1 += wm[m] * g1;
+                        sA2 += wa[m] * g2; sM2 += wm[m] * g2;
+                    }
+                    float c_last  = ws[OFF_C + b * Ln + Ln - 1];
+                    float wd_last = ws[OFF_WDCUM + b * Ln + Ln - 1];
+                    float mc_last = ws[OFF_MOMCUM + b * Ln + Ln - 1];
+                    p.out[OUT_B1P + b * 256 + t]  = sA1 - c_last * p.mb1[b * 256 + t] + wd_last * p.b1[b * 256 + t];
+                    p.out[OUT_MGB1 + b * 256 + t] = sM1 - mc_last * p.mb1[b * 256 + t];
+                    p.out[OUT_B2P + b * 256 + t]  = sA2 - c_last * p.mb2[b * 256 + t] + wd_last * p.b2[b * 256 + t];
+                    p.out[OUT_MGB2 + b * 256 + t] = sM2 - mc_last * p.mb2[b * 256 + t];
+                }
+                __syncthreads();
+            }
+        } else if (ph == 5) {
+            for (int u = blockIdx.x; u < 160; u += gridDim.x) {
+                if (u < 32) {
+                    int b = u >> 4; int l0 = (u & 15) * 8;
+                    score_unit(p, smem, t, b, l0, OFF_XQ, OFF_X2T, OFF_P2);
+                } else {
+                    int w = u - 32;
+                    int tt = w >> 2, ct = (w >> 1) & 1, mat = w & 1;
+                    int bl0 = tt * 8, c0 = ct * 128, b = bl0 >> 7;
+                    float (*xs)[260] = (float (*)[260])smem;
+                    stage8(ws + OFF_XQ + bl0 * 256, xs, t);
+                    __syncthreads();
+                    int tok = t >> 5, q = t & 31;
+                    int c = c0 + 4 * q;
+                    const float* W = ws + (mat ? OFF_MW2T : OFF_W2T) + b * 65536 + c;
+                    const float* bias = (mat ? p.mb2 : p.b2) + b * 256 + c;
+                    float4 a = dot256(xs, tok, W, 256);
+                    float4 bb = *(const float4*)bias;
+                    a.x += bb.x; a.y += bb.y; a.z += bb.z; a.w += bb.w;
+                    *(float4*)(ws + (mat ? OFF_V2 : OFF_U2) + (bl0 + tok) * 256 + c) = a;
+                }
+                __syncthreads();
+            }
+        } else {
+            for (int u = blockIdx.x; u < 64; u += gridDim.x) {
+                int tt = u >> 1, ct = u & 1;
+                int b = tt >> 4, l0 = (tt & 15) * 8;
+                combine_unit(p, smem, t, b, l0, ct * 128, OFF_P2, OFF_GZ2,
+                             OFF_U2, OFF_V2, 0, p.out + OUT_ZQ2);
+                __syncthreads();
+            }
+        }
+    }
 }
 
 extern "C" void kernel_launch(void* const* d_in, const int* in_sizes, int n_in,
                               void* d_out, int out_size, void* d_ws, size_t ws_size,
                               hipStream_t stream) {
-    const float* x   = (const float*)d_in[0];
-    const float* Wq  = (const float*)d_in[1];
-    const float* bq  = (const float*)d_in[2];
-    const float* Wk  = (const float*)d_in[3];
-    const float* bk  = (const float*)d_in[4];
-    const float* Wv  = (const float*)d_in[5];
-    const float* bv  = (const float*)d_in[6];
-    const float* Wlr = (const float*)d_in[7];
-    const float* blr = (const float*)d_in[8];
-    const float* Wm  = (const float*)d_in[9];
-    const float* bm  = (const float*)d_in[10];
-    const float* Wd  = (const float*)d_in[11];
-    const float* bd  = (const float*)d_in[12];
-    const float* W1  = (const float*)d_in[13];
-    const float* b1  = (const float*)d_in[14];
-    const float* W2  = (const float*)d_in[15];
-    const float* b2  = (const float*)d_in[16];
-    const float* mW1 = (const float*)d_in[17];
-    const float* mb1 = (const float*)d_in[18];
-    const float* mW2 = (const float*)d_in[19];
-    const float* mb2 = (const float*)d_in[20];
-    float* ws  = (float*)d_ws;
-    float* out = (float*)d_out;
-
-    prep_kernel<<<672, 256, 0, stream>>>(x, Wq, bq, Wk, bk, Wv, bv,
-                                         Wlr, blr, Wm, bm, Wd, bd,
-                                         W1, W2, mW1, mW2, ws);
-    mid_kernel<<<352, 256, 0, stream>>>(W2, b1, b2, mb1, ws);
-    fin1_kernel<<<1090, 256, 0, stream>>>(W1, mW1, W2, mW2,
-                                          b1, mb1, b2, mb2, out, ws);
-    fin2_kernel<<<96, 256, 0, stream>>>(b2, mb2, ws);
-    fin3_kernel<<<64, 256, 0, stream>>>(out, ws);
-}
+    KParams p;
+    p.x   = (const float*)d_in[0];
+    p.Wq  = (const float*)d_in[1];  p.bq  = (const float*)d_in[2];
+    p.Wk  = (const float*)d_in[3];  p.bk  = (const float*)d_in[4];
+    p.Wv  = (const float*)d_in[5];  p.bv  = (const float*)d_in[6];
+    p.Wlr = (const float*)d_in[7];  p.blr = (const float*)d_in[8];
+    p.Wm  = (const float*)d_in[9];  p.bm  = (const float*)d_in[10];
+    p.Wd  = (const float*)d_in[11]; p.bd  = (const float*)d_in[12];
+    p.W1  = (const float*)d_in[13]; p.b1  = (const float*)d_in[14];
+    p.W2  = (const float*)d_in[15]; p.b2  = (const float*)d_in[16];
+    p.mW1 = (const float*)d_in[17]; p.mb1 = (const float*)d_in[18];
+    p.mW2 = (const float*)d_in[19]; p.mb2 = (const float*)d_in[20];
+    p.out = (float*)d_out;
+    p.ws  = (float*)d_ws;
+
+    static int nblk = 0;
+    static int coop = -1;
+    if (coop < 0) {
+        int ca = 0;
+        if (hipDeviceGetAttribute(&ca, hipDeviceAttributeCooperativeLaunch, 0) != hipSuccess)
+            ca = 0;
+        int perCU = 0;
+        if (hipOccupancyMaxActiveBlocksPerMultiprocessor(&perCU, mega_kernel, 256, 0) != hipSuccess
+            || perCU < 1)
+            perCU = 1;
+        int ncu = 0;
+        if (hipDeviceGetAttribute(&ncu, hipDeviceAttributeMultiprocessorCount, 0) != hipSuccess
+            || ncu <= 0)
+            ncu = 256;
+        long cap = (long)perCU * (long)ncu;
+        nblk = (int)(cap < 512 ? cap : 512);
+        if (nblk < 1) nblk = 1;
+        coop = ca;
+    }
+
+    if (coop == 1) {
+        int lo = 0, hi = 6;
+        void* args[3] = {(void*)&p, (void*)&lo, (void*)&hi};
+        hipError_t e = hipLaunchCooperativeKernel(mega_kernel, dim3(nblk), dim3(256),
+                                                  args, 0, stream);
+        if (e == hipSuccess) return;
+        coop = 0;
+    }
+    for (int ph = 0; ph <= 6; ++ph)
+        mega_kernel<<<512, 256, 0, stream>>>(p, ph, ph);
+}
```

Result: slower. 393.2 us (+81.7%).
